# Kernel optimization log

Measured on AMD Instinct MI355X. Metric: run time of the kernel, lower is better.

The kernel has to match this reference:

```python
import jax, jax.numpy as jnp
import numpy as np

GAMMA = 1.1
PC_MIN_XY, PC_MAX_XY = -75.2, 75.2


def setup_inputs() -> dict:
    key = jax.random.key(0)
    k1, k2, k3, k4, k5 = jax.random.split(key, 5)
    N, B, F = 200000, 256, 5
    # points: x,y in pc range, z in [-2,4], remaining features small
    xy = jax.random.uniform(k1, (N, 2), minval=PC_MIN_XY, maxval=PC_MAX_XY)
    z = jax.random.uniform(k2, (N, 1), minval=-2.0, maxval=4.0)
    feat = jax.random.normal(k3, (N, F - 3)) * 0.1
    cur_points = jnp.concatenate([xy, z, feat], axis=-1).astype(jnp.float32)
    # boxes: cx,cy,cz, dx,dy (sizes ~1..6 m), dz, heading
    centers = jax.random.uniform(k4, (B, 3), minval=PC_MIN_XY, maxval=PC_MAX_XY)
    sizes = jax.random.uniform(k5, (B, 3), minval=1.0, maxval=6.0)
    heading = jnp.zeros((B, 1), dtype=jnp.float32)
    cur_boxes = jnp.concatenate([centers, sizes, heading], axis=-1).astype(jnp.float32)
    return {"cur_points": cur_points, "cur_boxes": cur_boxes, "num_sample": 128}


def reference(cur_points, cur_boxes, num_sample):
    # cylindrical_pool: radius-mask + topk + gather (N >= num_sample, so no pad)
    # radii of cylinders: ||(dx,dy)/2|| * gamma  -> [B]
    cur_radiis = jnp.linalg.norm(cur_boxes[:, 3:5] * 0.5, axis=-1) * GAMMA
    # pairwise xy distance [B, N]
    dis = jnp.linalg.norm(cur_points[None, :, :2] - cur_boxes[:, None, :2], axis=-1)
    point_mask = (dis <= cur_radiis[:, None]).astype(cur_points.dtype)  # [B, N]
    # topk over 0/1 mask: in-radius points first (ties -> lowest index, like torch)
    sampled_mask, sampled_idx = jax.lax.top_k(point_mask, num_sample)  # [B, S]
    sampled_points = cur_points[sampled_idx]  # [B, S, F] gather
    sampled_points = jnp.where(sampled_mask[..., None] > 0, sampled_points, 0.0)
    return sampled_points
```

## Files before the change

kernel.cpp:

```cpp
#include <hip/hip_runtime.h>

#define GAMMA_F 1.1f
#define F_DIM 5
#define BOXG 8
#define MAX_NSEG 256

__global__ void pack_xy_boxes_kernel(const float* __restrict__ pts,
                                     const float* __restrict__ boxes,
                                     float2* __restrict__ xy,
                                     float4* __restrict__ bp, int N, int B) {
  if (blockIdx.x == gridDim.x - 1) {
    for (int b = threadIdx.x; b < B; b += blockDim.x) {
      const float* bx = boxes + b * 7;
      const float hdx = __fmul_rn(bx[3], 0.5f);
      const float hdy = __fmul_rn(bx[4], 0.5f);
      const float r = __fmul_rn(
          __fsqrt_rn(__fadd_rn(__fmul_rn(hdx, hdx), __fmul_rn(hdy, hdy))),
          GAMMA_F);
      const unsigned ru = __float_as_uint(r);
      const float rsucc = __uint_as_float(ru + 1u);
      const double m = ((double)r + (double)rsucc) * 0.5;
      const double m2 = m * m;
      const bool incl = ((ru & 1u) == 0u);
      const float c1 = (float)m2;
      const double c1d = (double)c1;
      const bool keep = incl ? (c1d <= m2) : (c1d < m2);
      const float smax =
          keep ? c1 : __uint_as_float(__float_as_uint(c1) - 1u);
      bp[b] = make_float4(bx[0], bx[1], smax, 0.0f);
    }
    return;
  }
  const int i = blockIdx.x * blockDim.x + threadIdx.x;
  if (i < N) {
    float2 p;
    p.x = pts[i * F_DIM + 0];
    p.y = pts[i * F_DIM + 1];
    xy[i] = p;
  }
}

template <int NWAVE>
__global__ void __launch_bounds__(NWAVE * 64) seg_compact8_kernel(
    const float4* __restrict__ xy4, const float4* __restrict__ bp,
    int* __restrict__ cnt, unsigned short* __restrict__ idx, int N, int S,
    int NSEG, int L, int NGRP) {
  const int lane = threadIdx.x & 63;
  const int wid = threadIdx.x >> 6;
  const int g = blockIdx.x * NWAVE + wid;
  const int seg = g / NGRP;
  const int grp = g % NGRP;
  const int box0 = grp * BOXG;

  float cx[BOXG], cy[BOXG], smax[BOXG];
#pragma unroll
  for (int b = 0; b < BOXG; ++b) {
    const float4 v = bp[box0 + b];
    cx[b] = v.x;
    cy[b] = v.y;
    smax[b] = v.z;
  }

  const int start = seg * L;
  const int end = min(start + L, N);
  const int npts = end - start;

  int c[BOXG];
#pragma unroll
  for (int b = 0; b < BOXG; ++b) c[b] = 0;

  const unsigned long long lt = (1ULL << lane) - 1ULL;
  const unsigned long long le = lt | (1ULL << lane);
  const size_t ibase = ((size_t)box0 * NSEG + seg) * S;
  const int base4 = start >> 1;

  const int nfull = (npts > 0) ? (npts / 128) : 0;
  for (int it = 0; it < nfull; ++it) {
    const float4 q = xy4[base4 + it * 64 + lane];
    const int rel = it * 128 + 2 * lane;
#pragma unroll
    for (int b = 0; b < BOXG; ++b) {
      const float dx0 = __fsub_rn(q.x, cx[b]);
      const float dy0 = __fsub_rn(q.y, cy[b]);
      const float s0 = __fadd_rn(__fmul_rn(dx0, dx0), __fmul_rn(dy0, dy0));
      const float dx1 = __fsub_rn(q.z, cx[b]);
      const float dy1 = __fsub_rn(q.w, cy[b]);
      const float s1 = __fadd_rn(__fmul_rn(dx1, dx1), __fmul_rn(dy1, dy1));
      const bool sel0 = (s0 <= smax[b]);
      const bool sel1 = (s1 <= smax[b]);
      const unsigned long long m0 = __ballot(sel0);
      const unsigned long long m1 = __ballot(sel1);
      if (m0 | m1) {
        const int r0 = c[b] + __popcll(m0 & lt) + __popcll(m1 & lt);
        const int r1 = c[b] + __popcll(m0 & le) + __popcll(m1 & lt);
        unsigned short* mp = idx + ibase + (size_t)b * NSEG * S;
        if (sel0 && r0 < S) mp[r0] = (unsigned short)rel;
        if (sel1 && r1 < S) mp[r1] = (unsigned short)(rel + 1);
        c[b] += __popcll(m0) + __popcll(m1);
      }
    }
  }

  const int relb = nfull * 128;
  if (relb < npts) {
    const int rel = relb + 2 * lane;
    float4 q = make_float4(0.f, 0.f, 0.f, 0.f);
    if (rel < npts) q = xy4[base4 + nfull * 64 + lane];
#pragma unroll
    for (int b = 0; b < BOXG; ++b) {
      const float dx0 = __fsub_rn(q.x, cx[b]);
      const float dy0 = __fsub_rn(q.y, cy[b]);
      const float s0 = __fadd_rn(__fmul_rn(dx0, dx0), __fmul_rn(dy0, dy0));
      const float dx1 = __fsub_rn(q.z, cx[b]);
      const float dy1 = __fsub_rn(q.w, cy[b]);
      const float s1 = __fadd_rn(__fmul_rn(dx1, dx1), __fmul_rn(dy1, dy1));
      const bool sel0 = (rel < npts) && (s0 <= smax[b]);
      const bool sel1 = (rel + 1 < npts) && (s1 <= smax[b]);
      const unsigned long long m0 = __ballot(sel0);
      const unsigned long long m1 = __ballot(sel1);
      if (m0 | m1) {
        const int r0 = c[b] + __popcll(m0 & lt) + __popcll(m1 & lt);
        const int r1 = c[b] + __popcll(m0 & le) + __popcll(m1 & lt);
        unsigned short* mp = idx + ibase + (size_t)b * NSEG * S;
        if (sel0 && r0 < S) mp[r0] = (unsigned short)rel;
        if (sel1 && r1 < S) mp[r1] = (unsigned short)(rel + 1);
        c[b] += __popcll(m0) + __popcll(m1);
      }
    }
  }

  if (lane == 0) {
#pragma unroll
    for (int b = 0; b < BOXG; ++b) cnt[(box0 + b) * NSEG + seg] = min(c[b], S);
  }
}

__global__ void __launch_bounds__(256) gather_kernel(
    const float* __restrict__ pts, const int* __restrict__ cnt,
    const unsigned short* __restrict__ idx, float* __restrict__ out, int N,
    int S, int NSEG, int L) {
  const int b = blockIdx.x;
  const int tid = threadIdx.x;
  const int lane = tid & 63;
  const int wid = tid >> 6;

  __shared__ int pfx[MAX_NSEG + 1];
  __shared__ int wtot[4];
  __shared__ int woff[4];

  int v = (tid < NSEG) ? cnt[b * NSEG + tid] : 0;
  int sv = v;
#pragma unroll
  for (int d = 1; d < 64; d <<= 1) {
    const int t = __shfl_up(sv, d, 64);
    if (lane >= d) sv += t;
  }
  if (lane == 63) wtot[wid] = sv;
  __syncthreads();
  if (tid == 0) {
    int a = 0;
#pragma unroll
    for (int w = 0; w < 4; ++w) {
      woff[w] = a;
      a += wtot[w];
    }
  }
  __syncthreads();
  const int incl = sv + woff[wid];
  if (tid < NSEG) pfx[tid + 1] = incl;
  if (tid == 0) pfx[0] = 0;
  __syncthreads();

  const int total = pfx[NSEG];
  if (tid < S) {
    float* o = out + ((size_t)b * S + tid) * F_DIM;
    if (tid < total) {
      int lo = 0, hi = NSEG - 1;
      while (lo < hi) {
        const int mid = (lo + hi + 1) >> 1;
        if (pfx[mid] <= tid) lo = mid;
        else hi = mid - 1;
      }
      const int s = lo;
      const int gi =
          s * L + (int)idx[((size_t)b * NSEG + s) * S + (tid - pfx[s])];
      const float* p = pts + (size_t)gi * F_DIM;
      o[0] = p[0];
      o[1] = p[1];
      o[2] = p[2];
      o[3] = p[3];
      o[4] = p[4];
    } else {
      o[0] = 0.0f;
      o[1] = 0.0f;
      o[2] = 0.0f;
      o[3] = 0.0f;
      o[4] = 0.0f;
    }
  }
}

template <int BLOCK>
__global__ void __launch_bounds__(BLOCK) voxel_sampler_fallback(
    const float* __restrict__ pts, const float* __restrict__ boxes,
    float* __restrict__ out, int N, int S) {
  constexpr int NW = BLOCK / 64;
  const int b = blockIdx.x;
  const int tid = threadIdx.x;
  const int lane = tid & 63;
  const int wid = tid >> 6;

  const float cx = boxes[b * 7 + 0];
  const float cy = boxes[b * 7 + 1];
  const float hdx = __fmul_rn(boxes[b * 7 + 3], 0.5f);
  const float hdy = __fmul_rn(boxes[b * 7 + 4], 0.5f);
  const float r = __fmul_rn(
      __fsqrt_rn(__fadd_rn(__fmul_rn(hdx, hdx), __fmul_rn(hdy, hdy))),
      GAMMA_F);

  __shared__ int s_wsum[NW];
  __shared__ int s_count;
  if (tid == 0) s_count = 0;
  __syncthreads();

  float* outb = out + (size_t)b * S * F_DIM;

  for (int base = 0; base < N; base += BLOCK) {
    const int i = base + tid;
    bool sel = false;
    float x = 0.0f, y = 0.0f;
    if (i < N) {
      x = pts[i * F_DIM + 0];
      y = pts[i * F_DIM + 1];
      const float ddx = __fsub_rn(x, cx);
      const float ddy = __fsub_rn(y, cy);
      const float dis =
          __fsqrt_rn(__fadd_rn(__fmul_rn(ddx, ddx), __fmul_rn(ddy, ddy)));
      sel = (dis <= r);
    }
    const unsigned long long m = __ballot(sel);
    if (lane == 0) s_wsum[wid] = __popcll(m);
    __syncthreads();
    const int cbase = s_count;
    int wbase = 0;
    int tot = 0;
#pragma unroll
    for (int w = 0; w < NW; ++w) {
      const int v = s_wsum[w];
      if (w < wid) wbase += v;
      tot += v;
    }
    const int pos = cbase + wbase + __popcll(m & ((1ULL << lane) - 1ULL));
    if (sel && pos < S) {
      float* o = outb + pos * F_DIM;
      o[0] = x;
      o[1] = y;
      o[2] = pts[i * F_DIM + 2];
      o[3] = pts[i * F_DIM + 3];
      o[4] = pts[i * F_DIM + 4];
    }
    __syncthreads();
    if (tid == 0) s_count = cbase + tot;
    __syncthreads();
    if (cbase + tot >= S) break;
  }

  __syncthreads();
  int cnt = s_count;
  if (cnt > S) cnt = S;
  for (int j = cnt * F_DIM + tid; j < S * F_DIM; j += BLOCK) outb[j] = 0.0f;
}

extern "C" void kernel_launch(void* const* d_in, const int* in_sizes, int n_in,
                              void* d_out, int out_size, void* d_ws,
                              size_t ws_size, hipStream_t stream) {
  const float* pts = (const float*)d_in[0];
  const float* boxes = (const float*)d_in[1];
  float* out = (float*)d_out;

  const int N = in_sizes[0] / F_DIM;
  const int B = in_sizes[1] / 7;
  const int S = out_size / (B * F_DIM);

  const int NSEG = 256;
  int L = ((N + NSEG - 1) / NSEG + 1) & ~1;
  const int NGRP = B / BOXG;
  constexpr int NWAVE = 4;

  const size_t sz_xy = (size_t)N * sizeof(float2);
  const size_t off_cnt = (sz_xy + 255) & ~(size_t)255;
  const size_t sz_cnt = (size_t)B * NSEG * sizeof(int);
  const size_t off_idx = (off_cnt + sz_cnt + 255) & ~(size_t)255;
  const size_t sz_idx = (size_t)B * NSEG * S * sizeof(unsigned short);
  const size_t off_bp = (off_idx + sz_idx + 255) & ~(size_t)255;
  const size_t sz_bp = (size_t)B * sizeof(float4);
  const size_t need = off_bp + sz_bp;

  const bool fast = (ws_size >= need) && (L <= 65534) && (B % BOXG == 0) &&
                    (S <= 256) && (NSEG <= MAX_NSEG) && (N % 2 == 0) &&
                    ((NSEG * NGRP) % NWAVE == 0) &&
                    ((size_t)L * NSEG >= (size_t)N);

  if (fast) {
    char* ws = (char*)d_ws;
    float2* xy = (float2*)ws;
    int* cnt = (int*)(ws + off_cnt);
    unsigned short* idx = (unsigned short*)(ws + off_idx);
    float4* bpar = (float4*)(ws + off_bp);

    const int packb = (N + 255) / 256 + 1;
    pack_xy_boxes_kernel<<<packb, 256, 0, stream>>>(pts, boxes, xy, bpar, N,
                                                    B);
    seg_compact8_kernel<NWAVE>
        <<<(NSEG * NGRP) / NWAVE, NWAVE * 64, 0, stream>>>(
            (const float4*)xy, bpar, cnt, idx, N, S, NSEG, L, NGRP);
    gather_kernel<<<B, 256, 0, stream>>>(pts, cnt, idx, out, N, S, NSEG, L);
  } else {
    voxel_sampler_fallback<1024><<<B, 1024, 0, stream>>>(pts, boxes, out, N,
                                                         S);
  }
}
```

Baseline: 27.73 us.

## Fuse xy/box packing into compaction kernel and prefetch strided point loads

Removes the separate pack kernel. The compaction kernel now reads x,y directly from the strided 5-float point array and computes the squared-radius thresholds per wave from the raw boxes. The main loop software-prefetches the next iteration's coordinates, and lane prefix counts switch to mbcnt intrinsics. This saves a kernel launch and the intermediate xy buffer round trip. In exchange, the point loads become strided and uncoalesced, and the box-threshold math (including doubles) is repeated by every wave.

New measurement: 25.90 us. 6.6% less time.

```diff
diff --git a/kernel.cpp b/kernel.cpp
--- a/kernel.cpp
+++ b/kernel.cpp
@@ -5,60 +5,43 @@
 #define BOXG 8
 #define MAX_NSEG 256
 
-__global__ void pack_xy_boxes_kernel(const float* __restrict__ pts,
-                                     const float* __restrict__ boxes,
-                                     float2* __restrict__ xy,
-                                     float4* __restrict__ bp, int N, int B) {
-  if (blockIdx.x == gridDim.x - 1) {
-    for (int b = threadIdx.x; b < B; b += blockDim.x) {
-      const float* bx = boxes + b * 7;
-      const float hdx = __fmul_rn(bx[3], 0.5f);
-      const float hdy = __fmul_rn(bx[4], 0.5f);
-      const float r = __fmul_rn(
-          __fsqrt_rn(__fadd_rn(__fmul_rn(hdx, hdx), __fmul_rn(hdy, hdy))),
-          GAMMA_F);
-      const unsigned ru = __float_as_uint(r);
-      const float rsucc = __uint_as_float(ru + 1u);
-      const double m = ((double)r + (double)rsucc) * 0.5;
-      const double m2 = m * m;
-      const bool incl = ((ru & 1u) == 0u);
-      const float c1 = (float)m2;
-      const double c1d = (double)c1;
-      const bool keep = incl ? (c1d <= m2) : (c1d < m2);
-      const float smax =
-          keep ? c1 : __uint_as_float(__float_as_uint(c1) - 1u);
-      bp[b] = make_float4(bx[0], bx[1], smax, 0.0f);
-    }
-    return;
-  }
-  const int i = blockIdx.x * blockDim.x + threadIdx.x;
-  if (i < N) {
-    float2 p;
-    p.x = pts[i * F_DIM + 0];
-    p.y = pts[i * F_DIM + 1];
-    xy[i] = p;
-  }
+__device__ __forceinline__ int prefix_lt(unsigned long long m) {
+  return __builtin_amdgcn_mbcnt_hi(
+      (unsigned)(m >> 32), __builtin_amdgcn_mbcnt_lo((unsigned)m, 0u));
 }
 
 template <int NWAVE>
 __global__ void __launch_bounds__(NWAVE * 64) seg_compact8_kernel(
-    const float4* __restrict__ xy4, const float4* __restrict__ bp,
+    const float* __restrict__ pts, const float* __restrict__ boxes,
     int* __restrict__ cnt, unsigned short* __restrict__ idx, int N, int S,
     int NSEG, int L, int NGRP) {
   const int lane = threadIdx.x & 63;
   const int wid = threadIdx.x >> 6;
   const int g = blockIdx.x * NWAVE + wid;
   const int seg = g / NGRP;
-  const int grp = g % NGRP;
+  const int grp = g - seg * NGRP;
   const int box0 = grp * BOXG;
 
   float cx[BOXG], cy[BOXG], smax[BOXG];
 #pragma unroll
   for (int b = 0; b < BOXG; ++b) {
-    const float4 v = bp[box0 + b];
-    cx[b] = v.x;
-    cy[b] = v.y;
-    smax[b] = v.z;
+    const float* bx = boxes + (box0 + b) * 7;
+    cx[b] = bx[0];
+    cy[b] = bx[1];
+    const float hdx = __fmul_rn(bx[3], 0.5f);
+    const float hdy = __fmul_rn(bx[4], 0.5f);
+    const float r = __fmul_rn(
+        __fsqrt_rn(__fadd_rn(__fmul_rn(hdx, hdx), __fmul_rn(hdy, hdy))),
+        GAMMA_F);
+    const unsigned ru = __float_as_uint(r);
+    const float rsucc = __uint_as_float(ru + 1u);
+    const double m = ((double)r + (double)rsucc) * 0.5;
+    const double m2 = m * m;
+    const bool incl = ((ru & 1u) == 0u);
+    const float c1 = (float)m2;
+    const double c1d = (double)c1;
+    const bool keep = incl ? (c1d <= m2) : (c1d < m2);
+    smax[b] = keep ? c1 : __uint_as_float(__float_as_uint(c1) - 1u);
   }
 
   const int start = seg * L;
@@ -69,65 +52,71 @@
 #pragma unroll
   for (int b = 0; b < BOXG; ++b) c[b] = 0;
 
-  const unsigned long long lt = (1ULL << lane) - 1ULL;
-  const unsigned long long le = lt | (1ULL << lane);
   const size_t ibase = ((size_t)box0 * NSEG + seg) * S;
-  const int base4 = start >> 1;
-
   const int nfull = (npts > 0) ? (npts / 128) : 0;
-  for (int it = 0; it < nfull; ++it) {
-    const float4 q = xy4[base4 + it * 64 + lane];
-    const int rel = it * 128 + 2 * lane;
-#pragma unroll
-    for (int b = 0; b < BOXG; ++b) {
-      const float dx0 = __fsub_rn(q.x, cx[b]);
-      const float dy0 = __fsub_rn(q.y, cy[b]);
-      const float s0 = __fadd_rn(__fmul_rn(dx0, dx0), __fmul_rn(dy0, dy0));
-      const float dx1 = __fsub_rn(q.z, cx[b]);
-      const float dy1 = __fsub_rn(q.w, cy[b]);
-      const float s1 = __fadd_rn(__fmul_rn(dx1, dx1), __fmul_rn(dy1, dy1));
-      const bool sel0 = (s0 <= smax[b]);
-      const bool sel1 = (s1 <= smax[b]);
-      const unsigned long long m0 = __ballot(sel0);
-      const unsigned long long m1 = __ballot(sel1);
-      if (m0 | m1) {
-        const int r0 = c[b] + __popcll(m0 & lt) + __popcll(m1 & lt);
-        const int r1 = c[b] + __popcll(m0 & le) + __popcll(m1 & lt);
-        unsigned short* mp = idx + ibase + (size_t)b * NSEG * S;
-        if (sel0 && r0 < S) mp[r0] = (unsigned short)rel;
-        if (sel1 && r1 < S) mp[r1] = (unsigned short)(rel + 1);
-        c[b] += __popcll(m0) + __popcll(m1);
-      }
-    }
+
+  const float* pp = pts + (size_t)(start + 2 * lane) * F_DIM;
+
+#define PROCESS_8(RELBASE, X0, Y0, X1, Y1, G0, G1)                          \
+  {                                                                         \
+    const int rel = (RELBASE) + 2 * lane;                                   \
+    _Pragma("unroll") for (int b = 0; b < BOXG; ++b) {                      \
+      const float dx0 = __fsub_rn((X0), cx[b]);                             \
+      const float dy0 = __fsub_rn((Y0), cy[b]);                             \
+      const float s0 = __fadd_rn(__fmul_rn(dx0, dx0), __fmul_rn(dy0, dy0)); \
+      const float dx1 = __fsub_rn((X1), cx[b]);                             \
+      const float dy1 = __fsub_rn((Y1), cy[b]);                             \
+      const float s1 = __fadd_rn(__fmul_rn(dx1, dx1), __fmul_rn(dy1, dy1)); \
+      const bool sel0 = (G0) && (s0 <= smax[b]);                            \
+      const bool sel1 = (G1) && (s1 <= smax[b]);                            \
+      const unsigned long long m0 = __ballot(sel0);                         \
+      const unsigned long long m1 = __ballot(sel1);                         \
+      if (m0 | m1) {                                                        \
+        const int p0 = prefix_lt(m0);                                       \
+        const int p1 = prefix_lt(m1);                                       \
+        const int r0 = c[b] + p0 + p1;                                      \
+        const int r1 = c[b] + p0 + (sel0 ? 1 : 0) + p1;                     \
+        unsigned short* mp = idx + ibase + (size_t)b * NSEG * S;            \
+        if (sel0 && r0 < S) mp[r0] = (unsigned short)rel;                   \
+        if (sel1 && r1 < S) mp[r1] = (unsigned short)(rel + 1);             \
+        c[b] += __popcll(m0) + __popcll(m1);                                \
+      }                                                                     \
+    }                                                                       \
+  }
+
+  if (nfull > 0) {
+    float x0 = pp[0], y0 = pp[1], x1 = pp[5], y1 = pp[6];
+    for (int it = 0; it + 1 < nfull; ++it) {
+      const float* pn = pp + 128 * F_DIM;
+      const float nx0 = pn[0], ny0 = pn[1], nx1 = pn[5], ny1 = pn[6];
+      PROCESS_8(it * 128, x0, y0, x1, y1, true, true);
+      x0 = nx0;
+      y0 = ny0;
+      x1 = nx1;
+      y1 = ny1;
+      pp = pn;
+    }
+    PROCESS_8((nfull - 1) * 128, x0, y0, x1, y1, true, true);
+    pp += 128 * F_DIM;
   }
 
   const int relb = nfull * 128;
   if (relb < npts) {
     const int rel = relb + 2 * lane;
-    float4 q = make_float4(0.f, 0.f, 0.f, 0.f);
-    if (rel < npts) q = xy4[base4 + nfull * 64 + lane];
-#pragma unroll
-    for (int b = 0; b < BOXG; ++b) {
-      const float dx0 = __fsub_rn(q.x, cx[b]);
-      const float dy0 = __fsub_rn(q.y, cy[b]);
-      const float s0 = __fadd_rn(__fmul_rn(dx0, dx0), __fmul_rn(dy0, dy0));
-      const float dx1 = __fsub_rn(q.z, cx[b]);
-      const float dy1 = __fsub_rn(q.w, cy[b]);
-      const float s1 = __fadd_rn(__fmul_rn(dx1, dx1), __fmul_rn(dy1, dy1));
-      const bool sel0 = (rel < npts) && (s0 <= smax[b]);
-      const bool sel1 = (rel + 1 < npts) && (s1 <= smax[b]);
-      const unsigned long long m0 = __ballot(sel0);
-      const unsigned long long m1 = __ballot(sel1);
-      if (m0 | m1) {
-        const int r0 = c[b] + __popcll(m0 & lt) + __popcll(m1 & lt);
-        const int r1 = c[b] + __popcll(m0 & le) + __popcll(m1 & lt);
-        unsigned short* mp = idx + ibase + (size_t)b * NSEG * S;
-        if (sel0 && r0 < S) mp[r0] = (unsigned short)rel;
-        if (sel1 && r1 < S) mp[r1] = (unsigned short)(rel + 1);
-        c[b] += __popcll(m0) + __popcll(m1);
-      }
-    }
-  }
+    float x0 = 0.f, y0 = 0.f, x1 = 0.f, y1 = 0.f;
+    const bool g0 = (rel < npts);
+    const bool g1 = (rel + 1 < npts);
+    if (g0) {
+      x0 = pp[0];
+      y0 = pp[1];
+    }
+    if (g1) {
+      x1 = pp[5];
+      y1 = pp[6];
+    }
+    PROCESS_8(relb, x0, y0, x1, y1, g0, g1);
+  }
+#undef PROCESS_8
 
   if (lane == 0) {
 #pragma unroll
@@ -287,33 +276,24 @@
   const int NGRP = B / BOXG;
   constexpr int NWAVE = 4;
 
-  const size_t sz_xy = (size_t)N * sizeof(float2);
-  const size_t off_cnt = (sz_xy + 255) & ~(size_t)255;
   const size_t sz_cnt = (size_t)B * NSEG * sizeof(int);
-  const size_t off_idx = (off_cnt + sz_cnt + 255) & ~(size_t)255;
+  const size_t off_idx = (sz_cnt + 255) & ~(size_t)255;
   const size_t sz_idx = (size_t)B * NSEG * S * sizeof(unsigned short);
-  const size_t off_bp = (off_idx + sz_idx + 255) & ~(size_t)255;
-  const size_t sz_bp = (size_t)B * sizeof(float4);
-  const size_t need = off_bp + sz_bp;
-
-  const bool fast = (ws_size >= need) && (L <= 65534) && (B % BOXG == 0) &&
-                    (S <= 256) && (NSEG <= MAX_NSEG) && (N % 2 == 0) &&
-                    ((NSEG * NGRP) % NWAVE == 0) &&
+  const size_t need = off_idx + sz_idx;
+
+  const bool fast = (ws_size >= need) && (L >= 2) && (L - 1 <= 65535) &&
+                    (B % BOXG == 0) && (S <= 256) && (NSEG <= MAX_NSEG) &&
+                    ((NSEG * NGRP) % NWAVE == 0) && (NWAVE <= NGRP) &&
                     ((size_t)L * NSEG >= (size_t)N);
 
   if (fast) {
     char* ws = (char*)d_ws;
-    float2* xy = (float2*)ws;
-    int* cnt = (int*)(ws + off_cnt);
+    int* cnt = (int*)ws;
     unsigned short* idx = (unsigned short*)(ws + off_idx);
-    float4* bpar = (float4*)(ws + off_bp);
-
-    const int packb = (N + 255) / 256 + 1;
-    pack_xy_boxes_kernel<<<packb, 256, 0, stream>>>(pts, boxes, xy, bpar, N,
-                                                    B);
+
     seg_compact8_kernel<NWAVE>
         <<<(NSEG * NGRP) / NWAVE, NWAVE * 64, 0, stream>>>(
-            (const float4*)xy, bpar, cnt, idx, N, S, NSEG, L, NGRP);
+            pts, boxes, cnt, idx, N, S, NSEG, L, NGRP);
     gather_kernel<<<B, 256, 0, stream>>>(pts, cnt, idx, out, N, S, NSEG, L);
   } else {
     voxel_sampler_fallback<1024><<<B, 1024, 0, stream>>>(pts, boxes, out, N,
```
